# Kernel optimization log

Measured on AMD Instinct MI355X. Metric: run time of the kernel, lower is better.

## Reference

```python
import jax, jax.numpy as jnp
import numpy as np

B, S, H, E, TOP_K = 4, 4096, 4096, 64, 2

def setup_inputs() -> dict:
    key = jax.random.key(0)
    k1, k2 = jax.random.split(key)
    hidden_states = jax.random.normal(k1, (B, S, H), dtype=jnp.float32)
    gate_weight = jax.random.normal(k2, (E, H), dtype=jnp.float32) * (H ** -0.5)
    return {"hidden_states": hidden_states, "gate_weight": gate_weight}

def reference(hidden_states, gate_weight):
    # gate: logits[b,s,e] = hidden[b,s,h] @ W[e,h]^T (nn.Linear, no bias)
    router_logits = jnp.einsum('bsh,eh->bse', hidden_states, gate_weight)
    router_probs = jax.nn.softmax(router_logits, axis=-1)
    # top-k over experts, then renormalize the selected weights
    expert_weights, expert_indices = jax.lax.top_k(router_probs, TOP_K)
    expert_weights = expert_weights / jnp.sum(expert_weights, axis=-1, keepdims=True)
    return (router_probs, expert_indices, expert_weights)
```

## Files before the change

kernel.cpp:

```cpp
#include <hip/hip_runtime.h>
#include <math.h>

#define TOKENS 16384
#define HDIM 4096
#define NE 64

#define BM 64
#define LP 68

typedef float f32x4 __attribute__((ext_vector_type(4)));
typedef int i32x4 __attribute__((ext_vector_type(4)));
typedef __bf16 bf16x8 __attribute__((ext_vector_type(8)));

__device__ __forceinline__ void split8(f32x4 v0, f32x4 v1, i32x4& h, i32x4& l) {
  float x[8];
#pragma unroll
  for (int j = 0; j < 4; ++j) { x[j] = v0[j]; x[4 + j] = v1[j]; }
  union { unsigned short u[8]; i32x4 v; } H, L;
#pragma unroll
  for (int j = 0; j < 8; ++j) {
    __bf16 hb = (__bf16)x[j];
    H.u[j] = __builtin_bit_cast(unsigned short, hb);
    L.u[j] = __builtin_bit_cast(unsigned short, (__bf16)(x[j] - (float)hb));
  }
  h = H.v; l = L.v;
}

__device__ __forceinline__ f32x4 mfma_bf16(i32x4 a, i32x4 b, f32x4 c) {
  return __builtin_amdgcn_mfma_f32_16x16x32_bf16(
      __builtin_bit_cast(bf16x8, a), __builtin_bit_cast(bf16x8, b), c, 0, 0, 0);
}

__global__ __launch_bounds__(256) void convert_w(const float* __restrict__ W,
                                                 unsigned short* __restrict__ Wh,
                                                 unsigned short* __restrict__ Wl) {
  const int i = (blockIdx.x * 256 + threadIdx.x) * 8;
  f32x4 v0 = *(const f32x4*)(W + i);
  f32x4 v1 = *(const f32x4*)(W + i + 4);
  i32x4 h, l;
  split8(v0, v1, h, l);
  *(i32x4*)(Wh + i) = h;
  *(i32x4*)(Wl + i) = l;
}

__global__ __launch_bounds__(512, 2) void router_mfma(const float* __restrict__ A,
                                                      const unsigned short* __restrict__ Wh,
                                                      const unsigned short* __restrict__ Wl,
                                                      float* __restrict__ out) {
  __shared__ __align__(16) float L[BM * LP];

  const int tid = threadIdx.x;
  const int bt = blockIdx.x;
  const int lane = tid & 63;
  const int wv = tid >> 6;
  const int tg = wv & 3;
  const int eg = wv >> 2;
  const int l15 = lane & 15;
  const int fko = lane >> 4;

  const float* Ap = A + (size_t)(bt * BM + tg * 16 + l15) * HDIM + fko * 8;
  const unsigned short* Wh0 = Wh + (size_t)(eg * 32 + l15) * HDIM + fko * 8;
  const unsigned short* Wl0 = Wl + (size_t)(eg * 32 + l15) * HDIM + fko * 8;
  const unsigned short* Wh1 = Wh0 + 16 * HDIM;
  const unsigned short* Wl1 = Wl0 + 16 * HDIM;

  f32x4 acc0 = {0.f, 0.f, 0.f, 0.f};
  f32x4 acc1 = {0.f, 0.f, 0.f, 0.f};

#pragma unroll 2
  for (int kc = 0; kc < HDIM; kc += 32) {
    f32x4 a0 = *(const f32x4*)(Ap + kc);
    f32x4 a1 = *(const f32x4*)(Ap + kc + 4);
    i32x4 wh0 = *(const i32x4*)(Wh0 + kc);
    i32x4 wh1 = *(const i32x4*)(Wh1 + kc);
    i32x4 wl0 = *(const i32x4*)(Wl0 + kc);
    i32x4 wl1 = *(const i32x4*)(Wl1 + kc);
    i32x4 ah, al;
    split8(a0, a1, ah, al);
    acc0 = mfma_bf16(ah, wh0, acc0);
    acc1 = mfma_bf16(ah, wh1, acc1);
    acc0 = mfma_bf16(al, wh0, acc0);
    acc1 = mfma_bf16(al, wh1, acc1);
    acc0 = mfma_bf16(ah, wl0, acc0);
    acc1 = mfma_bf16(ah, wl1, acc1);
  }

#pragma unroll
  for (int r = 0; r < 4; ++r) {
    const int row = tg * 16 + fko * 4 + r;
    L[row * LP + eg * 32 + l15] = acc0[r];
    L[row * LP + eg * 32 + 16 + l15] = acc1[r];
  }
  __syncthreads();

  const int wv8 = tid >> 6;
#pragma unroll
  for (int r = 0; r < 8; ++r) {
    const int lt = wv8 * 8 + r;
    const int tok = bt * BM + lt;
    const float l = L[lt * LP + lane];

    float m = l;
#pragma unroll
    for (int off = 32; off >= 1; off >>= 1) m = fmaxf(m, __shfl_xor(m, off, 64));

    const float e = expf(l - m);
    float sum = e;
#pragma unroll
    for (int off = 32; off >= 1; off >>= 1) sum += __shfl_xor(sum, off, 64);

    const float p = e / sum;
    out[(size_t)tok * NE + lane] = p;

    float m0 = p;
#pragma unroll
    for (int off = 32; off >= 1; off >>= 1) m0 = fmaxf(m0, __shfl_xor(m0, off, 64));
    const unsigned long long b0 = __ballot(p == m0);
    const int i0 = __ffsll(b0) - 1;

    const float pm = (lane == i0) ? -1.f : p;
    float m1 = pm;
#pragma unroll
    for (int off = 32; off >= 1; off >>= 1) m1 = fmaxf(m1, __shfl_xor(m1, off, 64));
    const unsigned long long b1 = __ballot(pm == m1);
    const int i1 = __ffsll(b1) - 1;

    if (lane == 0) {
      float* idxo = out + (size_t)TOKENS * NE + (size_t)tok * 2;
      idxo[0] = (float)i0;
      idxo[1] = (float)i1;
      float* wo = out + (size_t)TOKENS * NE + (size_t)TOKENS * 2 + (size_t)tok * 2;
      const float d = m0 + m1;
      wo[0] = m0 / d;
      wo[1] = m1 / d;
    }
  }
}

extern "C" void kernel_launch(void* const* d_in, const int* in_sizes, int n_in,
                              void* d_out, int out_size, void* d_ws, size_t ws_size,
                              hipStream_t stream) {
  const float* A = (const float*)d_in[0];
  const float* W = (const float*)d_in[1];
  float* out = (float*)d_out;
  unsigned short* Whi = (unsigned short*)d_ws;
  unsigned short* Wlo = Whi + (size_t)NE * HDIM;

  convert_w<<<dim3(NE * HDIM / (256 * 8)), 256, 0, stream>>>(W, Whi, Wlo);
  router_mfma<<<dim3(TOKENS / BM), 512, 0, stream>>>(A, Whi, Wlo, out);
}
```

Before: 476.4 us.

## Split-K router GEMM with per-wave K slicing and separate softmax/top-k finalize kernel

The fused router kernel is replaced by a split-K GEMM. Each block handles 32 tokens and half of the hidden dimension, and its four waves take interleaved K chunks. The activations are split into bf16 hi/lo parts once per element and staged through LDS, so the split is no longer repeated per expert group, and the next chunk's loads are register-prefetched. Per-wave partial logits are reduced in LDS and written to a workspace, and a separate finalize kernel sums the K slices and does softmax and top-2. The aim is more parallelism and less redundant conversion work, at the cost of an extra kernel launch, partial-sum traffic to global memory, and serialized LDS reductions.

```diff
diff --git a/kernel.cpp b/kernel.cpp
--- a/kernel.cpp
+++ b/kernel.cpp
@@ -5,8 +5,14 @@
 #define HDIM 4096
 #define NE 64
 
-#define BM 64
-#define LP 68
+#define BMT 32
+#define BK 32
+#define KSPLIT 2
+#define KSLICE (HDIM / KSPLIT)
+#define NT (KSLICE / BK)
+#define WP 40
+#define AREG (BMT * WP)
+#define LPAD 68
 
 typedef float f32x4 __attribute__((ext_vector_type(4)));
 typedef int i32x4 __attribute__((ext_vector_type(4)));
@@ -43,97 +49,159 @@
   *(i32x4*)(Wl + i) = l;
 }
 
-__global__ __launch_bounds__(512, 2) void router_mfma(const float* __restrict__ A,
+__global__ __launch_bounds__(256, 4) void router_gemm(const float* __restrict__ A,
                                                       const unsigned short* __restrict__ Wh,
                                                       const unsigned short* __restrict__ Wl,
-                                                      float* __restrict__ out) {
-  __shared__ __align__(16) float L[BM * LP];
+                                                      float* __restrict__ P) {
+  __shared__ __align__(16) unsigned short smem[4 * 2 * AREG];
 
   const int tid = threadIdx.x;
   const int bt = blockIdx.x;
+  const int ks = blockIdx.y;
   const int lane = tid & 63;
   const int wv = tid >> 6;
-  const int tg = wv & 3;
-  const int eg = wv >> 2;
+
+  const int srow = lane >> 1;
+  const int sh = lane & 1;
+  const float* Ab = A + (size_t)(bt * BMT + srow) * HDIM + ks * KSLICE + sh * 16;
+
+  unsigned short* AhS = smem + wv * 2 * AREG;
+  unsigned short* AlS = AhS + AREG;
+  const int soff = srow * WP + sh * 16;
+
   const int l15 = lane & 15;
   const int fko = lane >> 4;
-
-  const float* Ap = A + (size_t)(bt * BM + tg * 16 + l15) * HDIM + fko * 8;
-  const unsigned short* Wh0 = Wh + (size_t)(eg * 32 + l15) * HDIM + fko * 8;
-  const unsigned short* Wl0 = Wl + (size_t)(eg * 32 + l15) * HDIM + fko * 8;
-  const unsigned short* Wh1 = Wh0 + 16 * HDIM;
-  const unsigned short* Wl1 = Wl0 + 16 * HDIM;
-
-  f32x4 acc0 = {0.f, 0.f, 0.f, 0.f};
-  f32x4 acc1 = {0.f, 0.f, 0.f, 0.f};
-
-#pragma unroll 2
-  for (int kc = 0; kc < HDIM; kc += 32) {
-    f32x4 a0 = *(const f32x4*)(Ap + kc);
-    f32x4 a1 = *(const f32x4*)(Ap + kc + 4);
-    i32x4 wh0 = *(const i32x4*)(Wh0 + kc);
-    i32x4 wh1 = *(const i32x4*)(Wh1 + kc);
-    i32x4 wl0 = *(const i32x4*)(Wl0 + kc);
-    i32x4 wl1 = *(const i32x4*)(Wl1 + kc);
-    i32x4 ah, al;
-    split8(a0, a1, ah, al);
-    acc0 = mfma_bf16(ah, wh0, acc0);
-    acc1 = mfma_bf16(ah, wh1, acc1);
-    acc0 = mfma_bf16(al, wh0, acc0);
-    acc1 = mfma_bf16(al, wh1, acc1);
-    acc0 = mfma_bf16(ah, wl0, acc0);
-    acc1 = mfma_bf16(ah, wl1, acc1);
-  }
-
-#pragma unroll
-  for (int r = 0; r < 4; ++r) {
-    const int row = tg * 16 + fko * 4 + r;
-    L[row * LP + eg * 32 + l15] = acc0[r];
-    L[row * LP + eg * 32 + 16 + l15] = acc1[r];
-  }
+  const unsigned short* Whp = Wh + (size_t)l15 * HDIM + ks * KSLICE + fko * 8;
+  const unsigned short* Wlp = Wl + (size_t)l15 * HDIM + ks * KSLICE + fko * 8;
+
+  f32x4 acc[2][4];
+#pragma unroll
+  for (int m = 0; m < 2; ++m)
+#pragma unroll
+    for (int e = 0; e < 4; ++e) acc[m][e] = (f32x4){0.f, 0.f, 0.f, 0.f};
+
+  f32x4 rc[4], rn[4];
+
+  auto loadA = [&](int s, f32x4* r) {
+    const int kc = (wv + 4 * s) * BK;
+#pragma unroll
+    for (int i = 0; i < 4; ++i) r[i] = *(const f32x4*)(Ab + kc + 4 * i);
+  };
+
+  loadA(0, rc);
+
+  for (int s = 0; s < NT / 4; ++s) {
+    const int kc = (wv + 4 * s) * BK;
+
+    i32x4 h0, l0, h1, l1;
+    split8(rc[0], rc[1], h0, l0);
+    split8(rc[2], rc[3], h1, l1);
+    *(i32x4*)&AhS[soff] = h0;
+    *(i32x4*)&AhS[soff + 8] = h1;
+    *(i32x4*)&AlS[soff] = l0;
+    *(i32x4*)&AlS[soff + 8] = l1;
+
+    const bool more = (s + 1 < NT / 4);
+    if (more) loadA(s + 1, rn);
+
+    i32x4 fah[2], fal[2];
+#pragma unroll
+    for (int m = 0; m < 2; ++m) {
+      const int off = (m * 16 + l15) * WP + fko * 8;
+      fah[m] = *(const i32x4*)&AhS[off];
+      fal[m] = *(const i32x4*)&AlS[off];
+    }
+
+#pragma unroll
+    for (int e = 0; e < 4; ++e) {
+      i32x4 fwh = *(const i32x4*)(Whp + (size_t)e * 16 * HDIM + kc);
+      i32x4 fwl = *(const i32x4*)(Wlp + (size_t)e * 16 * HDIM + kc);
+#pragma unroll
+      for (int m = 0; m < 2; ++m) {
+        acc[m][e] = mfma_bf16(fah[m], fwh, acc[m][e]);
+        acc[m][e] = mfma_bf16(fal[m], fwh, acc[m][e]);
+        acc[m][e] = mfma_bf16(fah[m], fwl, acc[m][e]);
+      }
+    }
+
+    if (more) {
+#pragma unroll
+      for (int i = 0; i < 4; ++i) rc[i] = rn[i];
+    }
+  }
+
   __syncthreads();
-
-  const int wv8 = tid >> 6;
-#pragma unroll
-  for (int r = 0; r < 8; ++r) {
-    const int lt = wv8 * 8 + r;
-    const int tok = bt * BM + lt;
-    const float l = L[lt * LP + lane];
-
-    float m = l;
-#pragma unroll
-    for (int off = 32; off >= 1; off >>= 1) m = fmaxf(m, __shfl_xor(m, off, 64));
-
-    const float e = expf(l - m);
-    float sum = e;
-#pragma unroll
-    for (int off = 32; off >= 1; off >>= 1) sum += __shfl_xor(sum, off, 64);
-
-    const float p = e / sum;
-    out[(size_t)tok * NE + lane] = p;
-
-    float m0 = p;
-#pragma unroll
-    for (int off = 32; off >= 1; off >>= 1) m0 = fmaxf(m0, __shfl_xor(m0, off, 64));
-    const unsigned long long b0 = __ballot(p == m0);
-    const int i0 = __ffsll(b0) - 1;
-
-    const float pm = (lane == i0) ? -1.f : p;
-    float m1 = pm;
-#pragma unroll
-    for (int off = 32; off >= 1; off >>= 1) m1 = fmaxf(m1, __shfl_xor(m1, off, 64));
-    const unsigned long long b1 = __ballot(pm == m1);
-    const int i1 = __ffsll(b1) - 1;
-
-    if (lane == 0) {
-      float* idxo = out + (size_t)TOKENS * NE + (size_t)tok * 2;
-      idxo[0] = (float)i0;
-      idxo[1] = (float)i1;
-      float* wo = out + (size_t)TOKENS * NE + (size_t)TOKENS * 2 + (size_t)tok * 2;
-      const float d = m0 + m1;
-      wo[0] = m0 / d;
-      wo[1] = m1 / d;
-    }
+  float* L = (float*)smem;
+#pragma unroll
+  for (int w = 0; w < 4; ++w) {
+    if (wv == w) {
+#pragma unroll
+      for (int m = 0; m < 2; ++m)
+#pragma unroll
+        for (int e = 0; e < 4; ++e)
+#pragma unroll
+          for (int r = 0; r < 4; ++r) {
+            const int idx = (m * 16 + fko * 4 + r) * LPAD + e * 16 + l15;
+            L[idx] = (w == 0) ? acc[m][e][r] : L[idx] + acc[m][e][r];
+          }
+    }
+    __syncthreads();
+  }
+
+  float* Pb = P + ((size_t)ks * TOKENS + (size_t)bt * BMT) * NE;
+  const int rr = tid >> 3;
+  const int cc = (tid & 7) * 8;
+#pragma unroll
+  for (int i = 0; i < 2; ++i) {
+    f32x4 v = *(const f32x4*)&L[rr * LPAD + cc + 4 * i];
+    *(f32x4*)&Pb[(size_t)rr * NE + cc + 4 * i] = v;
+  }
+}
+
+__global__ __launch_bounds__(256) void router_finalize(const float* __restrict__ P,
+                                                       float* __restrict__ out) {
+  const int lane = threadIdx.x & 63;
+  const int wave = threadIdx.x >> 6;
+  const int tok = blockIdx.x * 4 + wave;
+
+  float l = 0.f;
+#pragma unroll
+  for (int s = 0; s < KSPLIT; ++s)
+    l += P[((size_t)s * TOKENS + tok) * NE + lane];
+
+  float m = l;
+#pragma unroll
+  for (int off = 32; off >= 1; off >>= 1) m = fmaxf(m, __shfl_xor(m, off, 64));
+
+  const float e = expf(l - m);
+  float sum = e;
+#pragma unroll
+  for (int off = 32; off >= 1; off >>= 1) sum += __shfl_xor(sum, off, 64);
+
+  const float p = e / sum;
+  out[(size_t)tok * NE + lane] = p;
+
+  float m0 = p;
+#pragma unroll
+  for (int off = 32; off >= 1; off >>= 1) m0 = fmaxf(m0, __shfl_xor(m0, off, 64));
+  const unsigned long long b0 = __ballot(p == m0);
+  const int i0 = __ffsll(b0) - 1;
+
+  const float pm = (lane == i0) ? -1.f : p;
+  float m1 = pm;
+#pragma unroll
+  for (int off = 32; off >= 1; off >>= 1) m1 = fmaxf(m1, __shfl_xor(m1, off, 64));
+  const unsigned long long b1 = __ballot(pm == m1);
+  const int i1 = __ffsll(b1) - 1;
+
+  if (lane == 0) {
+    float* idxo = out + (size_t)TOKENS * NE + (size_t)tok * 2;
+    idxo[0] = (float)i0;
+    idxo[1] = (float)i1;
+    float* wo = out + (size_t)TOKENS * NE + (size_t)TOKENS * 2 + (size_t)tok * 2;
+    const float d = m0 + m1;
+    wo[0] = m0 / d;
+    wo[1] = m1 / d;
   }
 }
 
@@ -145,7 +213,9 @@
   float* out = (float*)d_out;
   unsigned short* Whi = (unsigned short*)d_ws;
   unsigned short* Wlo = Whi + (size_t)NE * HDIM;
+  float* P = (float*)(Wlo + (size_t)NE * HDIM);
 
   convert_w<<<dim3(NE * HDIM / (256 * 8)), 256, 0, stream>>>(W, Whi, Wlo);
-  router_mfma<<<dim3(TOKENS / BM), 512, 0, stream>>>(A, Whi, Wlo, out);
-}
+  router_gemm<<<dim3(TOKENS / BMT, KSPLIT), 256, 0, stream>>>(A, Whi, Wlo, P);
+  router_finalize<<<dim3(TOKENS / 4), 256, 0, stream>>>(P, out);
+}
```

Result: faster. 396.4 us (-16.8%).
